# Kernel tuning notes

Measured on AMD Instinct MI355X. Metric: run time of the kernel, lower is better.

The kernel has to match this reference:

```python
import jax, jax.numpy as jnp
import numpy as np

DIM = 256
RADIUS = 3
DIAM = 2 * RADIUS + 1          # 7
NNEIGH = DIAM * DIAM           # 49
B, H, W = 2, 64, 64
EPS_LN = 1e-6
EPS_NORM = 1e-7


def conv1x1(x, w, b):
    # x: [B,Cin,H,W], w: [Cout,Cin], b: [Cout]
    return jnp.einsum('oi,bihw->bohw', w, x) + b[None, :, None, None]


def layernorm2d(x, g, b):
    # channel-wise norm as in LayerNorm2d (mean/var over channel dim)
    u = x.mean(1, keepdims=True)
    s = ((x - u) ** 2).mean(1, keepdims=True)
    xn = (x - u) / jnp.sqrt(s + EPS_LN)
    return g[None, :, None, None] * xn + b[None, :, None, None]


def unfold_reflect(x, r):
    # torch F.unfold(pad(x, reflect, r), kernel=2r+1).reshape(B,C,D*D,H,W)
    d = 2 * r + 1
    hh, ww = x.shape[2], x.shape[3]
    xp = jnp.pad(x, ((0, 0), (0, 0), (r, r), (r, r)), mode='reflect')
    pats = [xp[:, :, i:i + hh, j:j + ww] for i in range(d) for j in range(d)]
    return jnp.stack(pats, axis=2)  # [B,C,D*D,H,W]


def setup_inputs() -> dict:
    key = jax.random.key(0)
    ks = jax.random.split(key, 20)
    sc_c = 1.0 / np.sqrt(DIM)
    sc_f = 1.0 / np.sqrt(NNEIGH + DIM)
    inp = {
        'spatial_feats': jax.random.normal(ks[0], (B, DIM, H, W), jnp.float32),
        'semantic_feats': jax.random.normal(ks[1], (B, DIM, H, W), jnp.float32),
        # range_proj: conv1x1 -> LN2d -> SiLU -> conv1x1
        'rp_w1': jax.random.normal(ks[2], (DIM, DIM), jnp.float32) * sc_c,
        'rp_b1': jnp.zeros((DIM,), jnp.float32),
        'rp_g': jnp.ones((DIM,), jnp.float32),
        'rp_be': jnp.zeros((DIM,), jnp.float32),
        'rp_w2': jax.random.normal(ks[3], (DIM, DIM), jnp.float32) * sc_c,
        'rp_b2': jnp.zeros((DIM,), jnp.float32),
        # fixup_proj: conv1x1(49+C->49) -> LN2d -> SiLU -> conv1x1(49->49)
        'fp_w1': jax.random.normal(ks[4], (NNEIGH, NNEIGH + DIM), jnp.float32) * sc_f,
        'fp_b1': jnp.zeros((NNEIGH,), jnp.float32),
        'fp_g': jnp.ones((NNEIGH,), jnp.float32),
        'fp_be': jnp.zeros((NNEIGH,), jnp.float32),
        'fp_w2': jax.random.normal(ks[5], (NNEIGH, NNEIGH), jnp.float32) * (1.0 / np.sqrt(NNEIGH)),
        'fp_b2': jnp.zeros((NNEIGH,), jnp.float32),
        # output_proj: conv1x1 -> LN2d -> conv1x1
        'op_w1': jax.random.normal(ks[6], (DIM, DIM), jnp.float32) * sc_c,
        'op_b1': jnp.zeros((DIM,), jnp.float32),
        'op_g': jnp.ones((DIM,), jnp.float32),
        'op_be': jnp.zeros((DIM,), jnp.float32),
        'op_w2': jax.random.normal(ks[7], (DIM, DIM), jnp.float32) * sc_c,
        'op_b2': jnp.zeros((DIM,), jnp.float32),
        'sigma_spatial': jnp.ones((), jnp.float32),
    }
    return inp


def reference(spatial_feats, semantic_feats,
              rp_w1, rp_b1, rp_g, rp_be, rp_w2, rp_b2,
              fp_w1, fp_b1, fp_g, fp_be, fp_w2, fp_b2,
              op_w1, op_b1, op_g, op_be, op_w2, op_b2,
              sigma_spatial):
    scale = jnp.asarray(DIM ** 0.5, spatial_feats.dtype)
    # range_proj(semantic_feats)
    px = conv1x1(semantic_feats, rp_w1, rp_b1)
    px = jax.nn.silu(layernorm2d(px, rp_g, rp_be))
    px = conv1x1(px, rp_w2, rp_b2)  # [B,C,H,W]

    # spatial (Gaussian) kernel over the window
    lin = jnp.linspace(-1.0, 1.0, DIAM)
    xg, yg = jnp.meshgrid(lin, lin, indexing='ij')
    spatial_kernel = jnp.exp(-(xg ** 2 + yg ** 2) / (2.0 * sigma_spatial ** 2))
    spatial_kernel = spatial_kernel.reshape(1, NNEIGH, 1, 1)

    # range kernel: local similarity + softmax over the 49 neighbors
    queries = unfold_reflect(px, RADIUS)                       # [B,C,N,H,W]
    sim = jnp.einsum('bcnhw,bchw->bnhw', queries, px) / scale
    range_kernel = jax.nn.softmax(sim.astype(jnp.float32), axis=1).astype(px.dtype)

    # neighborhoods of spatial features
    neighborhoods = unfold_reflect(spatial_feats, RADIUS)      # [B,C,N,H,W]

    # gated fixup correction
    ck = range_kernel * spatial_kernel                          # [B,N,H,W]
    fx = conv1x1(jnp.concatenate([ck, semantic_feats], axis=1), fp_w1, fp_b1)
    fx = jax.nn.silu(layernorm2d(fx, fp_g, fp_be))
    fx = conv1x1(fx, fp_w2, fp_b2)
    ck = ck + ck * jax.nn.sigmoid(fx)
    ck = ck / (ck.sum(1, keepdims=True) + EPS_NORM)

    # weighted neighborhood sum
    out = jnp.einsum('bcnhw,bnhw->bchw', neighborhoods, ck)

    # output_proj (note: no SiLU here, matching the module)
    out = conv1x1(out, op_w1, op_b1)
    out = layernorm2d(out, op_g, op_be)
    out = conv1x1(out, op_w2, op_b2)
    return out
```

## Files before the change

### kernel.cpp

```cpp
#include <hip/hip_runtime.h>
#include <cstdint>

#define HW 4096
#define C_ 256
#define NN 49
#define KW 305

typedef __bf16 bf16;
typedef bf16 bf16x8 __attribute__((ext_vector_type(8)));
typedef bf16 bf16x4 __attribute__((ext_vector_type(4)));
typedef float f32x4 __attribute__((ext_vector_type(4)));

#define GLD16(src, dst) __builtin_amdgcn_global_load_lds( \
    (const __attribute__((address_space(1))) uint32_t*)(src), \
    (__attribute__((address_space(3))) uint32_t*)(dst), 16, 0, 0)

__device__ __forceinline__ int refl(int i) { return i < 0 ? -i : (i > 63 ? 126 - i : i); }
__device__ __forceinline__ float sigmoidf_(float x) { return 1.f / (1.f + __expf(-x)); }

__global__ __launch_bounds__(256) void setup_k(const float* __restrict__ spatial,
                                               const float* __restrict__ semantic,
                                               const float* __restrict__ rp_w1,
                                               const float* __restrict__ rp_w2,
                                               const float* __restrict__ op_w1,
                                               const float* __restrict__ op_w2,
                                               const float* __restrict__ fp_w1,
                                               const float* __restrict__ fp_w2,
                                               const float* __restrict__ sigma,
                                               bf16* __restrict__ spb, bf16* __restrict__ seb,
                                               bf16* __restrict__ wrp1, bf16* __restrict__ wrp2,
                                               bf16* __restrict__ wop1, bf16* __restrict__ wop2,
                                               bf16* __restrict__ w1ckb, bf16* __restrict__ w1sb,
                                               bf16* __restrict__ w2Tg, float* __restrict__ sk)
{
    __shared__ float tile[32][33];
    const int bid = blockIdx.x, t = threadIdx.x;
    if (bid < 4096) {
        int z = bid >> 10, r = bid & 1023;
        int b = z & 1;
        const float* src = (z >> 1) ? semantic : spatial;
        bf16* dst = (z >> 1) ? seb : spb;
        int p0 = (r & 127) * 32, c0 = (r >> 7) * 32;
        int tx = t & 31, ty = t >> 5;
        const float* s = src + (size_t)b * C_ * HW;
        #pragma unroll
        for (int i = 0; i < 32; i += 8)
            tile[ty + i][tx] = s[(size_t)(c0 + ty + i) * HW + p0 + tx];
        __syncthreads();
        int p = t >> 3, cq = (t & 7) * 4;
        bf16x4 o = {(bf16)tile[cq][p], (bf16)tile[cq + 1][p], (bf16)tile[cq + 2][p], (bf16)tile[cq + 3][p]};
        *(bf16x4*)&dst[((size_t)b * HW + p0 + p) * C_ + c0 + cq] = o;
        return;
    }
    int pid = bid - 4096;
    if (pid < 256) {
        const float* src = (pid < 64) ? rp_w1 : (pid < 128) ? rp_w2 : (pid < 192) ? op_w1 : op_w2;
        bf16* dst = (pid < 64) ? wrp1 : (pid < 128) ? wrp2 : (pid < 192) ? wop1 : wop2;
        int i = ((pid & 63) * 256 + t) * 4;
        f32x4 v = *(const f32x4*)&src[i];
        bf16x4 o = {(bf16)v[0], (bf16)v[1], (bf16)v[2], (bf16)v[3]};
        *(bf16x4*)&dst[i] = o;
    } else if (pid == 256) {
        if (t < NN) {
            int i = t / 7, j = t % 7;
            float xg = (i - 3) * (1.f / 3.f), yg = (j - 3) * (1.f / 3.f);
            float s = sigma[0];
            sk[t] = __expf(-(xg * xg + yg * yg) / (2.f * s * s));
        }
    } else if (pid < 270) {
        int idx = (pid - 257) * 256 + t;
        if (idx < NN * 64) {
            int k = idx >> 6, o = idx & 63;
            w1ckb[idx] = (o < NN) ? (bf16)fp_w1[o * KW + k] : (bf16)0.f;
        }
    } else if (pid < 334) {
        int idx = (pid - 270) * 256 + t;
        int o = idx >> 8, c = idx & 255;
        w1sb[idx] = (o < NN) ? (bf16)fp_w1[o * KW + NN + c] : (bf16)0.f;
    } else {
        int idx = (pid - 334) * 256 + t;
        if (idx < NN * 64) {
            int k = idx >> 6, o = idx & 63;
            w2Tg[idx] = (o < NN) ? (bf16)fp_w2[o * NN + k] : (bf16)0.f;
        }
    }
}

__device__ __forceinline__ void stage_b(const bf16* __restrict__ Wp, bf16* dst, int kc, int t)
{
    const bf16* gB = Wp + (size_t)(t >> 2) * C_ + kc + (((t & 3) ^ ((t >> 3) & 3)) * 8);
    #pragma unroll
    for (int ii = 0; ii < 4; ++ii)
        GLD16(gB + (size_t)ii * 64 * C_, dst + ii * 2048 + t * 8);
}

template<bool SILU, int MODE>
__global__ __launch_bounds__(256) void conv_pair(const bf16* __restrict__ X,
                                                 const bf16* __restrict__ W1,
                                                 const float* __restrict__ b1v,
                                                 const float* __restrict__ g,
                                                 const float* __restrict__ be,
                                                 const bf16* __restrict__ W2,
                                                 const float* __restrict__ b2v,
                                                 void* __restrict__ Yv)
{
    __shared__ __align__(16) bf16 Xf[32 * 256];
    __shared__ __align__(16) bf16 Mid[32 * 256];
    __shared__ __align__(16) bf16 Bs[2][256 * 32];
    __shared__ float lnred[32][4][2];
    const int t = threadIdx.x;
    const int lane = t & 63, wc = t >> 6;
    const int l15 = lane & 15, kb = lane >> 4;
    const long q0 = (long)blockIdx.x * 32;

    {
        const int r8 = t >> 5, slot = t & 31;
        const bf16* gX = X + (q0 + r8) * C_ + ((slot ^ (r8 & 7)) * 8);
        #pragma unroll
        for (int i = 0; i < 4; ++i)
            GLD16(gX + (size_t)i * 8 * C_, &Xf[i * 2048 + t * 8]);
    }
    stage_b(W1, &Bs[0][0], 0, t);

    const int x7 = l15 & 7;
    const int bsl = (kb ^ ((l15 >> 1) & 3)) * 8;
    int boff[4];
    #pragma unroll
    for (int n = 0; n < 4; ++n)
        boff[n] = (wc * 64 + n * 16 + l15) * 32 + bsl;
    const int a0base = l15 * 256;
    const int a1base = (16 + l15) * 256;

    f32x4 acc[2][4];
    #pragma unroll
    for (int m = 0; m < 2; ++m)
        #pragma unroll
        for (int n = 0; n < 4; ++n) acc[m][n] = (f32x4){0.f, 0.f, 0.f, 0.f};

    __syncthreads();
    int cur = 0;
    #pragma unroll
    for (int ks = 0; ks < 8; ++ks) {
        if (ks < 7) stage_b(W1, &Bs[cur ^ 1][0], (ks + 1) * 32, t);
        const int ko = ((ks * 4 + kb) ^ x7) * 8;
        bf16x8 a0 = *(const bf16x8*)&Xf[a0base + ko];
        bf16x8 a1 = *(const bf16x8*)&Xf[a1base + ko];
        #pragma unroll
        for (int n = 0; n < 4; ++n) {
            bf16x8 b = *(const bf16x8*)&Bs[cur][boff[n]];
            acc[0][n] = __builtin_amdgcn_mfma_f32_16x16x32_bf16(a0, b, acc[0][n], 0, 0, 0);
            acc[1][n] = __builtin_amdgcn_mfma_f32_16x16x32_bf16(a1, b, acc[1][n], 0, 0, 0);
        }
        __syncthreads();
        cur ^= 1;
    }

    stage_b(W2, &Bs[0][0], 0, t);

    float s4[2][4], ss4[2][4];
    #pragma unroll
    for (int m = 0; m < 2; ++m)
        #pragma unroll
        for (int r = 0; r < 4; ++r) { s4[m][r] = 0.f; ss4[m][r] = 0.f; }
    #pragma unroll
    for (int n = 0; n < 4; ++n) {
        float bo = b1v[wc * 64 + n * 16 + l15];
        #pragma unroll
        for (int m = 0; m < 2; ++m)
            #pragma unroll
            for (int r = 0; r < 4; ++r) {
                float v = acc[m][n][r] + bo;
                acc[m][n][r] = v;
                s4[m][r] += v; ss4[m][r] += v * v;
            }
    }
    #pragma unroll
    for (int off = 1; off <= 8; off <<= 1)
        #pragma unroll
        for (int m = 0; m < 2; ++m)
            #pragma unroll
            for (int r = 0; r < 4; ++r) {
                s4[m][r]  += __shfl_xor(s4[m][r], off, 64);
                ss4[m][r] += __shfl_xor(ss4[m][r], off, 64);
            }
    if (l15 == 0) {
        #pragma unroll
        for (int m = 0; m < 2; ++m)
            #pragma unroll
            for (int r = 0; r < 4; ++r) {
                lnred[m * 16 + kb * 4 + r][wc][0] = s4[m][r];
                lnred[m * 16 + kb * 4 + r][wc][1] = ss4[m][r];
            }
    }
    __syncthreads();
    float mean[2][4], rstd[2][4];
    #pragma unroll
    for (int m = 0; m < 2; ++m)
        #pragma unroll
        for (int r = 0; r < 4; ++r) {
            int p = m * 16 + kb * 4 + r;
            float st  = lnred[p][0][0] + lnred[p][1][0] + lnred[p][2][0] + lnred[p][3][0];
            float sst = lnred[p][0][1] + lnred[p][1][1] + lnred[p][2][1] + lnred[p][3][1];
            mean[m][r] = st * (1.f / 256.f);
            float var = sst * (1.f / 256.f) - mean[m][r] * mean[m][r];
            rstd[m][r] = rsqrtf(var + 1e-6f);
        }
    #pragma unroll
    for (int n = 0; n < 4; ++n) {
        int ch = wc * 64 + n * 16 + l15;
        float gv = g[ch], bev = be[ch];
        #pragma unroll
        for (int m = 0; m < 2; ++m)
            #pragma unroll
            for (int r = 0; r < 4; ++r) {
                float y = (acc[m][n][r] - mean[m][r]) * rstd[m][r] * gv + bev;
                if (SILU) y *= sigmoidf_(y);
                int p = m * 16 + kb * 4 + r;
                Mid[p * 256 + (((ch >> 3) ^ (p & 7)) * 8) + (ch & 7)] = (bf16)y;
            }
    }
    __syncthreads();

    f32x4 acc2[2][4];
    #pragma unroll
    for (int m = 0; m < 2; ++m)
        #pragma unroll
        for (int n = 0; n < 4; ++n) acc2[m][n] = (f32x4){0.f, 0.f, 0.f, 0.f};
    cur = 0;
    #pragma unroll
    for (int ks = 0; ks < 8; ++ks) {
        if (ks < 7) stage_b(W2, &Bs[cur ^ 1][0], (ks + 1) * 32, t);
        const int ko = ((ks * 4 + kb) ^ x7) * 8;
        bf16x8 a0 = *(const bf16x8*)&Mid[a0base + ko];
        bf16x8 a1 = *(const bf16x8*)&Mid[a1base + ko];
        #pragma unroll
        for (int n = 0; n < 4; ++n) {
            bf16x8 b = *(const bf16x8*)&Bs[cur][boff[n]];
            acc2[0][n] = __builtin_amdgcn_mfma_f32_16x16x32_bf16(a0, b, acc2[0][n], 0, 0, 0);
            acc2[1][n] = __builtin_amdgcn_mfma_f32_16x16x32_bf16(a1, b, acc2[1][n], 0, 0, 0);
        }
        __syncthreads();
        cur ^= 1;
    }

    if constexpr (MODE == 0) {
        #pragma unroll
        for (int n = 0; n < 4; ++n) {
            int ch = wc * 64 + n * 16 + l15;
            float bo = b2v[ch];
            #pragma unroll
            for (int m = 0; m < 2; ++m)
                #pragma unroll
                for (int r = 0; r < 4; ++r)
                    Xf[(m * 16 + kb * 4 + r) * 256 + ch] = (bf16)(acc2[m][n][r] + bo);
        }
        __syncthreads();
        bf16* Y = (bf16*)Yv;
        const int p = t >> 3, cb = (t & 7) * 32;
        #pragma unroll
        for (int i = 0; i < 4; ++i) {
            bf16x8 v = *(const bf16x8*)&Xf[p * 256 + cb + i * 8];
            *(bf16x8*)&Y[(q0 + p) * C_ + cb + i * 8] = v;
        }
    } else {
        float* Y = (float*)Yv;
        const int bb = (int)(q0 >> 12);
        #pragma unroll
        for (int n = 0; n < 4; ++n) {
            int ch = wc * 64 + n * 16 + l15;
            float bo = b2v[ch];
            #pragma unroll
            for (int m = 0; m < 2; ++m) {
                int pp = (int)(q0 & 4095) + m * 16 + kb * 4;
                f32x4 val = {acc2[m][n][0] + bo, acc2[m][n][1] + bo,
                             acc2[m][n][2] + bo, acc2[m][n][3] + bo};
                *(f32x4*)&Y[((size_t)bb * C_ + ch) * HW + pp] = val;
            }
        }
    }
}

__global__ __launch_bounds__(256) void attn_out_k(const bf16* __restrict__ px,
                                                  const bf16* __restrict__ spb,
                                                  const bf16* __restrict__ seb,
                                                  const bf16* __restrict__ w1sb,
                                                  const bf16* __restrict__ w1ckb,
                                                  const bf16* __restrict__ w2Tg,
                                                  const float* __restrict__ b1,
                                                  const float* __restrict__ b2,
                                                  const float* __restrict__ g,
                                                  const float* __restrict__ be,
                                                  const float* __restrict__ sk,
                                                  const bf16* __restrict__ wop1,
                                                  const float* __restrict__ ob1,
                                                  const float* __restrict__ og,
                                                  const float* __restrict__ obe,
                                                  const bf16* __restrict__ wop2,
                                                  const float* __restrict__ ob2,
                                                  float* __restrict__ Y)
{
    __shared__ __align__(16) char shm[49664];
    bf16*  uni = (bf16*)(shm);
    float* ckl = (float*)(shm + 25600);
    float* hb  = (float*)(shm + 29760);
    float* S   = (float*)(shm + 32768);
    float* fxs = (float*)(shm + 40384);
    bf16*  Xg  = (bf16*)(shm + 32768);
    bf16*  Mid = (bf16*)(shm + 40960);
    bf16*  Bs0 = (bf16*)(shm);
    bf16*  Bs1 = (bf16*)(shm + 16384);
    float* lnred = (float*)(shm + 49152);

    const int t = threadIdx.x, lane = t & 63, wid = t >> 6;
    const int l15 = lane & 15, kb = lane >> 4;
    const int blk = blockIdx.x;
    const int batch = blk >> 8, tt = blk & 255;
    const int h0 = (tt >> 4) * 4, w0 = (tt & 15) * 4;
    const long base = (long)batch * HW;

    const float bo  = (lane < NN) ? b1[lane] : 0.f;
    const float gl  = (lane < NN) ? g[lane] : 0.f;
    const float bel = (lane < NN) ? be[lane] : 0.f;
    const float b2l = (lane < NN) ? b2[lane] : 0.f;
    const float skv = (lane < NN) ? sk[lane] : 0.f;
    const int nn_ = (lane < NN) ? lane : 0;
    const int dy = nn_ / 7, dx = nn_ % 7;

#define STAGE_UNI(ci) do { \
    _Pragma("unroll") \
    for (int i_ = 0; i_ < 7; ++i_) { \
        int st_ = i_ * 256 + t; \
        if (st_ < 1600) { \
            int u_ = st_ >> 4, s_ = st_ & 15; \
            int uy_ = (u_ * 205) >> 11, ux_ = u_ - uy_ * 10; \
            long grow_ = base + refl(h0 + uy_ - 3) * 64 + refl(w0 + ux_ - 3); \
            GLD16(spb + grow_ * C_ + (ci) * 128 + ((s_ ^ (u_ & 7)) * 8), &uni[u_ * 128 + s_ * 8]); \
        } \
    } \
} while (0)

    STAGE_UNI(0);

    const int ppy = l15 >> 2, ppx = l15 & 3;
    const long qB = base + (h0 + ppy) * 64 + (w0 + ppx);
    const bf16* bpxp = px + qB * C_ + kb * 8;
    const bf16* bsemp = seb + qB * C_ + kb * 8;

    bool valid[3], ispx[3];
    const bf16* arow[3];
    #pragma unroll
    for (int j = 0; j < 3; ++j) {
        int tid = wid + 4 * j;
        valid[j] = tid < 11;
        ispx[j] = tid < 7;
        int u = tid * 16 + l15;
        int uy = (u * 205) >> 11, ux = u - uy * 10;
        long grow = (u < 100) ? base + refl(h0 + uy - 3) * 64 + refl(w0 + ux - 3) : base;
        int o = ((tid - 7) & 3) * 16 + l15;
        arow[j] = ispx[j] ? (px + grow * C_ + kb * 8)
                          : (w1sb + (size_t)o * C_ + kb * 8);
    }

    f32x4 acc[3];
    #pragma unroll
    for (int j = 0; j < 3; ++j) acc[j] = (f32x4){0.f, 0.f, 0.f, 0.f};

    #pragma unroll
    for (int ks = 0; ks < 8; ++ks) {
        bf16x8 bp = *(const bf16x8*)(bpxp + ks * 32);
        bf16x8 bs = *(const bf16x8*)(bsemp + ks * 32);
        #pragma unroll
        for (int j = 0; j < 3; ++j) {
            if (valid[j]) {
                bf16x8 a = *(const bf16x8*)(arow[j] + ks * 32);
                acc[j] = __builtin_amdgcn_mfma_f32_16x16x32_bf16(a, ispx[j] ? bp : bs, acc[j], 0, 0, 0);
            }
        }
    }

    float w1r[NN], w2r[NN];
    #pragma unroll
    for (int k = 0; k < NN; ++k) {
        w1r[k] = (float)w1ckb[k * 64 + lane];
        w2r[k] = (float)w2Tg[k * 64 + lane];
    }

    #pragma unroll
    for (int j = 0; j < 3; ++j) {
        if (valid[j]) {
            int tid = wid + 4 * j;
            float* dst = ispx[j] ? &S[(tid * 16 + kb * 4) * 17 + l15]
                                 : &fxs[(((tid - 7) * 16) + kb * 4) * 17 + l15];
            dst[0] = acc[j][0]; dst[17] = acc[j][1]; dst[34] = acc[j][2]; dst[51] = acc[j][3];
        }
    }
    __syncthreads();

    #pragma unroll
    for (int j = 0; j < 4; ++j) {
        int p = wid * 4 + j, py = p >> 2, px4 = p & 3;
        int u = (py + dy) * 10 + px4 + dx;
        float sval = (lane < NN) ? S[u * 17 + p] * 0.0625f : -1e30f;
        float mx = sval;
        #pragma unroll
        for (int off = 32; off; off >>= 1) mx = fmaxf(mx, __shfl_xor(mx, off, 64));
        float ev = (lane < NN) ? __expf(sval - mx) : 0.f;
        float ssum = ev;
        #pragma unroll
        for (int off = 32; off; off >>= 1) ssum += __shfl_xor(ssum, off, 64);
        ckl[p * 65 + lane] = (lane < NN) ? (ev / ssum) * skv : 0.f;
    }

    #pragma unroll
    for (int j = 0; j < 4; ++j) {
        int p = wid * 4 + j;
        float fxa = 0.f, fxb = 0.f;
        #pragma unroll
        for (int k = 0; k < 48; k += 2) {
            fxa += w1r[k] * ckl[p * 65 + k];
            fxb += w1r[k + 1] * ckl[p * 65 + k + 1];
        }
        fxa += w1r[48] * ckl[p * 65 + 48];
        float fx = fxs[lane * 17 + p] + bo + fxa + fxb;
        float s = fx, ss = fx * fx;
        #pragma unroll
        for (int off = 32; off; off >>= 1) {
            s  += __shfl_xor(s, off, 64);
            ss += __shfl_xor(ss, off, 64);
        }
        float mean = s * (1.f / 49.f);
        float var  = ss * (1.f / 49.f) - mean * mean;
        float rstd = rsqrtf(var + 1e-6f);
        float hv = 0.f;
        if (lane < NN) {
            float xn = (fx - mean) * rstd * gl + bel;
            hv = xn * sigmoidf_(xn);
        }
        hb[wid * 64 + lane] = hv;
        float ckv = 0.f;
        if (lane < NN) {
            float ca = 0.f, cb = 0.f;
            #pragma unroll
            for (int k = 0; k < 48; k += 2) {
                ca += w2r[k] * hb[wid * 64 + k];
                cb += w2r[k + 1] * hb[wid * 64 + k + 1];
            }
            ca += w2r[48] * hb[wid * 64 + 48];
            ckv = ckl[p * 65 + lane] * (1.f + sigmoidf_(b2l + ca + cb));
        }
        float tot = ckv;
        #pragma unroll
        for (int off = 32; off; off >>= 1) tot += __shfl_xor(tot, off, 64);
        ckl[p * 65 + lane] = (lane < NN) ? ckv / (tot + 1e-7f) : 0.f;
    }
    __syncthreads();

    const int sub = lane >> 4;
    const int gp = wid * 4 + sub;

    #pragma unroll
    for (int ci = 0; ci < 2; ++ci) {
        if (ci == 1) {
            __syncthreads();
            STAGE_UNI(1);
            __syncthreads();
        }
        const int ub = (gp >> 2) * 10 + (gp & 3);
        float a[8];
        #pragma unroll
        for (int e = 0; e < 8; ++e) a[e] = 0.f;
        for (int dyy = 0; dyy < 7; ++dyy) {
            bf16x8 v[7];
            #pragma unroll
            for (int dxx = 0; dxx < 7; ++dxx) {
                int u = ub + dyy * 10 + dxx;
                v[dxx] = *(const bf16x8*)&uni[u * 128 + ((l15 ^ (u & 7)) * 8)];
            }
            #pragma unroll
            for (int dxx = 0; dxx < 7; ++dxx) {
                float cv = ckl[gp * 65 + dyy * 7 + dxx];
                #pragma unroll
                for (int e = 0; e < 8; ++e) a[e] += cv * (float)v[dxx][e];
            }
        }
        bf16x8 ov;
        #pragma unroll
        for (int e = 0; e < 8; ++e) ov[e] = (bf16)a[e];
        *(bf16x8*)&Xg[gp * 256 + (((ci * 16 + l15) ^ (gp & 7)) * 8)] = ov;
    }
    __syncthreads();

    stage_b(wop1, Bs0, 0, t);

    const int x7 = l15 & 7;
    const int bsl = (kb ^ ((l15 >> 1) & 3)) * 8;
    int boff[4];
    #pragma unroll
    for (int n = 0; n < 4; ++n)
        boff[n] = (wid * 64 + n * 16 + l15) * 32 + bsl;

    f32x4 cacc[4];
    #pragma unroll
    for (int n = 0; n < 4; ++n) cacc[n] = (f32x4){0.f, 0.f, 0.f, 0.f};

    __syncthreads();
    int cur = 0;
    #pragma unroll
    for (int ks = 0; ks < 8; ++ks) {
        if (ks < 7) stage_b(wop1, cur ? Bs0 : Bs1, (ks + 1) * 32, t);
        const int ko = ((ks * 4 + kb) ^ x7) * 8;
        bf16x8 a = *(const bf16x8*)&Xg[l15 * 256 + ko];
        #pragma unroll
        for (int n = 0; n < 4; ++n) {
            bf16x8 b = *(const bf16x8*)&((cur ? Bs1 : Bs0)[boff[n]]);
            cacc[n] = __builtin_amdgcn_mfma_f32_16x16x32_bf16(a, b, cacc[n], 0, 0, 0);
        }
        __syncthreads();
        cur ^= 1;
    }

    stage_b(wop2, Bs0, 0, t);

    float s4[4] = {0.f, 0.f, 0.f, 0.f}, ss4[4] = {0.f, 0.f, 0.f, 0.f};
    #pragma unroll
    for (int n = 0; n < 4; ++n) {
        float bv = ob1[wid * 64 + n * 16 + l15];
        #pragma unroll
        for (int r = 0; r < 4; ++r) {
            float v = cacc[n][r] + bv;
            cacc[n][r] = v;
            s4[r] += v; ss4[r] += v * v;
        }
    }
    #pragma unroll
    for (int off = 1; off <= 8; off <<= 1)
        #pragma unroll
        for (int r = 0; r < 4; ++r) {
            s4[r]  += __shfl_xor(s4[r], off, 64);
            ss4[r] += __shfl_xor(ss4[r], off, 64);
        }
    if (l15 == 0) {
        #pragma unroll
        for (int r = 0; r < 4; ++r) {
            lnred[((kb * 4 + r) * 4 + wid) * 2 + 0] = s4[r];
            lnred[((kb * 4 + r) * 4 + wid) * 2 + 1] = ss4[r];
        }
    }
    __syncthreads();
    float mean[4], rstd[4];
    #pragma unroll
    for (int r = 0; r < 4; ++r) {
        int p = kb * 4 + r;
        float st  = lnred[(p * 4 + 0) * 2] + lnred[(p * 4 + 1) * 2] + lnred[(p * 4 + 2) * 2] + lnred[(p * 4 + 3) * 2];
        float sst = lnred[(p * 4 + 0) * 2 + 1] + lnred[(p * 4 + 1) * 2 + 1] + lnred[(p * 4 + 2) * 2 + 1] + lnred[(p * 4 + 3) * 2 + 1];
        mean[r] = st * (1.f / 256.f);
        float var = sst * (1.f / 256.f) - mean[r] * mean[r];
        rstd[r] = rsqrtf(var + 1e-6f);
    }
    #pragma unroll
    for (int n = 0; n < 4; ++n) {
        int ch = wid * 64 + n * 16 + l15;
        float gv = og[ch], bev = obe[ch];
        #pragma unroll
        for (int r = 0; r < 4; ++r) {
            float y = (cacc[n][r] - mean[r]) * rstd[r] * gv + bev;
            int p = kb * 4 + r;
            Mid[p * 256 + (((ch >> 3) ^ (p & 7)) * 8) + (ch & 7)] = (bf16)y;
        }
    }
    __syncthreads();

    f32x4 cacc2[4];
    #pragma unroll
    for (int n = 0; n < 4; ++n) cacc2[n] = (f32x4){0.f, 0.f, 0.f, 0.f};
    cur = 0;
    #pragma unroll
    for (int ks = 0; ks < 8; ++ks) {
        if (ks < 7) stage_b(wop2, cur ? Bs0 : Bs1, (ks + 1) * 32, t);
        const int ko = ((ks * 4 + kb) ^ x7) * 8;
        bf16x8 a = *(const bf16x8*)&Mid[l15 * 256 + ko];
        #pragma unroll
        for (int n = 0; n < 4; ++n) {
            bf16x8 b = *(const bf16x8*)&((cur ? Bs1 : Bs0)[boff[n]]);
            cacc2[n] = __builtin_amdgcn_mfma_f32_16x16x32_bf16(a, b, cacc2[n], 0, 0, 0);
        }
        __syncthreads();
        cur ^= 1;
    }

    {
        const size_t rowbase = ((size_t)batch * C_) * HW + (size_t)(h0 + kb) * 64 + w0;
        #pragma unroll
        for (int n = 0; n < 4; ++n) {
            int ch = wid * 64 + n * 16 + l15;
            float bv = ob2[ch];
            f32x4 val = {cacc2[n][0] + bv, cacc2[n][1] + bv, cacc2[n][2] + bv, cacc2[n][3] + bv};
            *(f32x4*)&Y[rowbase + (size_t)ch * HW] = val;
        }
    }
#undef STAGE_UNI
}

extern "C" void kernel_launch(void* const* d_in, const int* in_sizes, int n_in,
                              void* d_out, int out_size, void* d_ws, size_t ws_size,
                              hipStream_t stream)
{
    const float* spatial  = (const float*)d_in[0];
    const float* semantic = (const float*)d_in[1];
    const float* rp_w1 = (const float*)d_in[2];
    const float* rp_b1 = (const float*)d_in[3];
    const float* rp_g  = (const float*)d_in[4];
    const float* rp_be = (const float*)d_in[5];
    const float* rp_w2 = (const float*)d_in[6];
    const float* rp_b2 = (const float*)d_in[7];
    const float* fp_w1 = (const float*)d_in[8];
    const float* fp_b1 = (const float*)d_in[9];
    const float* fp_g  = (const float*)d_in[10];
    const float* fp_be = (const float*)d_in[11];
    const float* fp_w2 = (const float*)d_in[12];
    const float* fp_b2 = (const float*)d_in[13];
    const float* op_w1 = (const float*)d_in[14];
    const float* op_b1 = (const float*)d_in[15];
    const float* op_g  = (const float*)d_in[16];
    const float* op_be = (const float*)d_in[17];
    const float* op_w2 = (const float*)d_in[18];
    const float* op_b2 = (const float*)d_in[19];
    const float* sigma = (const float*)d_in[20];

    const size_t NPX = 2 * (size_t)HW;
    float* ws = (float*)d_ws;
    float* sk    = ws;
    bf16* bfbase = (bf16*)(sk + 64);
    bf16* spb = bfbase;
    bf16* seb = spb + NPX * C_;
    bf16* t1  = seb + NPX * C_;
    bf16* wrp1 = t1 + NPX * C_;
    bf16* wrp2 = wrp1 + C_ * C_;
    bf16* wop1 = wrp2 + C_ * C_;
    bf16* wop2 = wop1 + C_ * C_;
    bf16* w1sb = wop2 + C_ * C_;
    bf16* w2Tg = w1sb + 64 * C_;
    bf16* w1ckb = w2Tg + 3200;

    setup_k<<<4443, 256, 0, stream>>>(spatial, semantic, rp_w1, rp_w2, op_w1, op_w2,
                                      fp_w1, fp_w2, sigma,
                                      spb, seb, wrp1, wrp2, wop1, wop2,
                                      w1ckb, w1sb, w2Tg, sk);

    conv_pair<true, 0><<<256, 256, 0, stream>>>(seb, wrp1, rp_b1, rp_g, rp_be, wrp2, rp_b2, t1);

    attn_out_k<<<512, 256, 0, stream>>>(t1, spb, seb, w1sb, w1ckb, w2Tg, fp_b1, fp_b2,
                                        fp_g, fp_be, sk,
                                        wop1, op_b1, op_g, op_be, wop2, op_b2,
                                        (float*)d_out);
}
```

Before: 65.74 us.

## Double attn_out_k block to 512 threads and read neighborhoods straight from global

The fused attention/output kernel now runs 8 waves per block instead of 4. Each wave handles half as many pixels and output-channel tiles. The fixup weights w1/w2 are staged into LDS instead of being held in 98 registers per thread, which lowers register pressure. The weighted neighborhood sum loads spatial features directly from global memory (relying on cache) instead of staging the 10x10 halo into LDS in two channel halves, which removes those staging passes and their barriers. In exchange it does more uncached-path global loads and pays for reductions across more waves.

Measured after the change: 70.59 us. +7.4%, slower.

```diff
diff --git a/kernel.cpp b/kernel.cpp
--- a/kernel.cpp
+++ b/kernel.cpp
@@ -94,6 +94,13 @@
         GLD16(gB + (size_t)ii * 64 * C_, dst + ii * 2048 + t * 8);
 }
 
+__device__ __forceinline__ void stage_b512(const bf16* __restrict__ Wp, bf16* dst, int kc, int t)
+{
+    const bf16* gB = Wp + (size_t)(t >> 2) * C_ + kc + (((t & 3) ^ ((t >> 3) & 3)) * 8);
+    GLD16(gB, dst + t * 8);
+    GLD16(gB + (size_t)128 * C_, dst + 4096 + t * 8);
+}
+
 template<bool SILU, int MODE>
 __global__ __launch_bounds__(256) void conv_pair(const bf16* __restrict__ X,
                                                  const bf16* __restrict__ W1,
@@ -280,39 +287,40 @@
     }
 }
 
-__global__ __launch_bounds__(256) void attn_out_k(const bf16* __restrict__ px,
-                                                  const bf16* __restrict__ spb,
-                                                  const bf16* __restrict__ seb,
-                                                  const bf16* __restrict__ w1sb,
-                                                  const bf16* __restrict__ w1ckb,
-                                                  const bf16* __restrict__ w2Tg,
-                                                  const float* __restrict__ b1,
-                                                  const float* __restrict__ b2,
-                                                  const float* __restrict__ g,
-                                                  const float* __restrict__ be,
-                                                  const float* __restrict__ sk,
-                                                  const bf16* __restrict__ wop1,
-                                                  const float* __restrict__ ob1,
-                                                  const float* __restrict__ og,
-                                                  const float* __restrict__ obe,
-                                                  const bf16* __restrict__ wop2,
-                                                  const float* __restrict__ ob2,
-                                                  float* __restrict__ Y)
+__global__ __launch_bounds__(512, 4) void attn_out_k(const bf16* __restrict__ px,
+                                                     const bf16* __restrict__ spb,
+                                                     const bf16* __restrict__ seb,
+                                                     const bf16* __restrict__ w1sb,
+                                                     const bf16* __restrict__ w1ckb,
+                                                     const bf16* __restrict__ w2Tg,
+                                                     const float* __restrict__ b1,
+                                                     const float* __restrict__ b2,
+                                                     const float* __restrict__ g,
+                                                     const float* __restrict__ be,
+                                                     const float* __restrict__ sk,
+                                                     const bf16* __restrict__ wop1,
+                                                     const float* __restrict__ ob1,
+                                                     const float* __restrict__ og,
+                                                     const float* __restrict__ obe,
+                                                     const bf16* __restrict__ wop2,
+                                                     const float* __restrict__ ob2,
+                                                     float* __restrict__ Y)
 {
-    __shared__ __align__(16) char shm[49664];
-    bf16*  uni = (bf16*)(shm);
-    float* ckl = (float*)(shm + 25600);
-    float* hb  = (float*)(shm + 29760);
-    float* S   = (float*)(shm + 32768);
-    float* fxs = (float*)(shm + 40384);
-    bf16*  Xg  = (bf16*)(shm + 32768);
-    bf16*  Mid = (bf16*)(shm + 40960);
-    bf16*  Bs0 = (bf16*)(shm);
-    bf16*  Bs1 = (bf16*)(shm + 16384);
-    float* lnred = (float*)(shm + 49152);
+    __shared__ __align__(16) char shm[56384];
+    float* ckl = (float*)(shm);
+    float* hb  = (float*)(shm + 4160);
+    float* S   = (float*)(shm + 6208);
+    float* fxs = (float*)(shm + 13824);
+    bf16*  w1l = (bf16*)(shm + 18176);
+    bf16*  w2l = (bf16*)(shm + 24448);
+    bf16*  Bs0 = (bf16*)(shm + 6208);
+    bf16*  Bs1 = (bf16*)(shm + 22592);
+    bf16*  Xg  = (bf16*)(shm + 38976);
+    bf16*  Mid = (bf16*)(shm + 47168);
+    float* lnred = (float*)(shm + 55360);
 
     const int t = threadIdx.x, lane = t & 63, wid = t >> 6;
-    const int l15 = lane & 15, kb = lane >> 4;
+    const int l15 = lane & 15, kb = lane >> 4, l31 = lane & 31;
     const int blk = blockIdx.x;
     const int batch = blk >> 8, tt = blk & 255;
     const int h0 = (tt >> 4) * 4, w0 = (tt & 15) * 4;
@@ -326,79 +334,52 @@
     const int nn_ = (lane < NN) ? lane : 0;
     const int dy = nn_ / 7, dx = nn_ % 7;
 
-#define STAGE_UNI(ci) do { \
-    _Pragma("unroll") \
-    for (int i_ = 0; i_ < 7; ++i_) { \
-        int st_ = i_ * 256 + t; \
-        if (st_ < 1600) { \
-            int u_ = st_ >> 4, s_ = st_ & 15; \
-            int uy_ = (u_ * 205) >> 11, ux_ = u_ - uy_ * 10; \
-            long grow_ = base + refl(h0 + uy_ - 3) * 64 + refl(w0 + ux_ - 3); \
-            GLD16(spb + grow_ * C_ + (ci) * 128 + ((s_ ^ (u_ & 7)) * 8), &uni[u_ * 128 + s_ * 8]); \
-        } \
-    } \
-} while (0)
-
-    STAGE_UNI(0);
+    if (t < 392) GLD16(w1ckb + (size_t)t * 8, &w1l[t * 8]);
+    if (t < 392) GLD16(w2Tg + (size_t)t * 8, &w2l[t * 8]);
 
     const int ppy = l15 >> 2, ppx = l15 & 3;
     const long qB = base + (h0 + ppy) * 64 + (w0 + ppx);
     const bf16* bpxp = px + qB * C_ + kb * 8;
     const bf16* bsemp = seb + qB * C_ + kb * 8;
 
-    bool valid[3], ispx[3];
-    const bf16* arow[3];
-    #pragma unroll
-    for (int j = 0; j < 3; ++j) {
-        int tid = wid + 4 * j;
-        valid[j] = tid < 11;
-        ispx[j] = tid < 7;
-        int u = tid * 16 + l15;
+    const bool t0sim = wid < 7;
+    const bool t1v = wid < 3;
+    const bf16* a0p;
+    {
+        int u = wid * 16 + l15;
         int uy = (u * 205) >> 11, ux = u - uy * 10;
         long grow = (u < 100) ? base + refl(h0 + uy - 3) * 64 + refl(w0 + ux - 3) : base;
-        int o = ((tid - 7) & 3) * 16 + l15;
-        arow[j] = ispx[j] ? (px + grow * C_ + kb * 8)
-                          : (w1sb + (size_t)o * C_ + kb * 8);
-    }
-
-    f32x4 acc[3];
-    #pragma unroll
-    for (int j = 0; j < 3; ++j) acc[j] = (f32x4){0.f, 0.f, 0.f, 0.f};
-
+        a0p = t0sim ? (px + grow * C_ + kb * 8)
+                    : (w1sb + (size_t)l15 * C_ + kb * 8);
+    }
+    const bf16* a1p = w1sb + (size_t)((wid + 1) * 16 + l15) * C_ + kb * 8;
+
+    f32x4 acc0 = {0.f, 0.f, 0.f, 0.f}, acc1 = {0.f, 0.f, 0.f, 0.f};
     #pragma unroll
     for (int ks = 0; ks < 8; ++ks) {
         bf16x8 bp = *(const bf16x8*)(bpxp + ks * 32);
         bf16x8 bs = *(const bf16x8*)(bsemp + ks * 32);
-        #pragma unroll
-        for (int j = 0; j < 3; ++j) {
-            if (valid[j]) {
-                bf16x8 a = *(const bf16x8*)(arow[j] + ks * 32);
-                acc[j] = __builtin_amdgcn_mfma_f32_16x16x32_bf16(a, ispx[j] ? bp : bs, acc[j], 0, 0, 0);
-            }
-        }
-    }
-
-    float w1r[NN], w2r[NN];
-    #pragma unroll
-    for (int k = 0; k < NN; ++k) {
-        w1r[k] = (float)w1ckb[k * 64 + lane];
-        w2r[k] = (float)w2Tg[k * 64 + lane];
-    }
-
-    #pragma unroll
-    for (int j = 0; j < 3; ++j) {
-        if (valid[j]) {
-            int tid = wid + 4 * j;
-            float* dst = ispx[j] ? &S[(tid * 16 + kb * 4) * 17 + l15]
-                                 : &fxs[(((tid - 7) * 16) + kb * 4) * 17 + l15];
-            dst[0] = acc[j][0]; dst[17] = acc[j][1]; dst[34] = acc[j][2]; dst[51] = acc[j][3];
-        }
-    }
-    __syncthreads();
-
-    #pragma unroll
-    for (int j = 0; j < 4; ++j) {
-        int p = wid * 4 + j, py = p >> 2, px4 = p & 3;
+        bf16x8 a0 = *(const bf16x8*)(a0p + ks * 32);
+        acc0 = __builtin_amdgcn_mfma_f32_16x16x32_bf16(a0, t0sim ? bp : bs, acc0, 0, 0, 0);
+        if (t1v) {
+            bf16x8 a1 = *(const bf16x8*)(a1p + ks * 32);
+            acc1 = __builtin_amdgcn_mfma_f32_16x16x32_bf16(a1, bs, acc1, 0, 0, 0);
+        }
+    }
+    {
+        float* dst = t0sim ? &S[(wid * 16 + kb * 4) * 17 + l15]
+                           : &fxs[(kb * 4) * 17 + l15];
+        dst[0] = acc0[0]; dst[17] = acc0[1]; dst[34] = acc0[2]; dst[51] = acc0[3];
+    }
+    if (t1v) {
+        float* dst = &fxs[((wid + 1) * 16 + kb * 4) * 17 + l15];
+        dst[0] = acc1[0]; dst[17] = acc1[1]; dst[34] = acc1[2]; dst[51] = acc1[3];
+    }
+    __syncthreads();
+
+    #pragma unroll
+    for (int j = 0; j < 2; ++j) {
+        int p = wid * 2 + j, py = p >> 2, px4 = p & 3;
         int u = (py + dy) * 10 + px4 + dx;
         float sval = (lane < NN) ? S[u * 17 + p] * 0.0625f : -1e30f;
         float mx = sval;
@@ -412,15 +393,15 @@
     }
 
     #pragma unroll
-    for (int j = 0; j < 4; ++j) {
-        int p = wid * 4 + j;
+    for (int j = 0; j < 2; ++j) {
+        int p = wid * 2 + j;
         float fxa = 0.f, fxb = 0.f;
         #pragma unroll
         for (int k = 0; k < 48; k += 2) {
-            fxa += w1r[k] * ckl[p * 65 + k];
-            fxb += w1r[k + 1] * ckl[p * 65 + k + 1];
-        }
-        fxa += w1r[48] * ckl[p * 65 + 48];
+            fxa += (float)w1l[k * 64 + lane] * ckl[p * 65 + k];
+            fxb += (float)w1l[(k + 1) * 64 + lane] * ckl[p * 65 + k + 1];
+        }
+        fxa += (float)w1l[48 * 64 + lane] * ckl[p * 65 + 48];
         float fx = fxs[lane * 17 + p] + bo + fxa + fxb;
         float s = fx, ss = fx * fx;
         #pragma unroll
@@ -442,10 +423,10 @@
             float ca = 0.f, cb = 0.f;
             #pragma unroll
             for (int k = 0; k < 48; k += 2) {
-                ca += w2r[k] * hb[wid * 64 + k];
-                cb += w2r[k + 1] * hb[wid * 64 + k + 1];
+                ca += (float)w2l[k * 64 + lane] * hb[wid * 64 + k];
+                cb += (float)w2l[(k + 1) * 64 + lane] * hb[wid * 64 + k + 1];
             }
-            ca += w2r[48] * hb[wid * 64 + 48];
+            ca += (float)w2l[48 * 64 + lane] * hb[wid * 64 + 48];
             ckv = ckl[p * 65 + lane] * (1.f + sigmoidf_(b2l + ca + cb));
         }
         float tot = ckv;
@@ -455,27 +436,27 @@
     }
     __syncthreads();
 
-    const int sub = lane >> 4;
-    const int gp = wid * 4 + sub;
-
-    #pragma unroll
-    for (int ci = 0; ci < 2; ++ci) {
-        if (ci == 1) {
-            __syncthreads();
-            STAGE_UNI(1);
-            __syncthreads();
-        }
-        const int ub = (gp >> 2) * 10 + (gp & 3);
+    stage_b512(wop1, Bs0, 0, t);
+
+    {
+        const int gp = wid * 2 + (lane >> 5);
+        const int gpy = gp >> 2, gpx = gp & 3;
+        int ry[7], rx[7];
+        #pragma unroll
+        for (int d = 0; d < 7; ++d) {
+            ry[d] = refl(h0 + gpy + d - 3) * 64;
+            rx[d] = refl(w0 + gpx + d - 3);
+        }
+        const bf16* pb = spb + base * C_ + l31 * 8;
         float a[8];
         #pragma unroll
         for (int e = 0; e < 8; ++e) a[e] = 0.f;
+        #pragma unroll
         for (int dyy = 0; dyy < 7; ++dyy) {
             bf16x8 v[7];
             #pragma unroll
-            for (int dxx = 0; dxx < 7; ++dxx) {
-                int u = ub + dyy * 10 + dxx;
-                v[dxx] = *(const bf16x8*)&uni[u * 128 + ((l15 ^ (u & 7)) * 8)];
-            }
+            for (int dxx = 0; dxx < 7; ++dxx)
+                v[dxx] = *(const bf16x8*)(pb + (size_t)(ry[dyy] + rx[dxx]) * C_);
             #pragma unroll
             for (int dxx = 0; dxx < 7; ++dxx) {
                 float cv = ckl[gp * 65 + dyy * 7 + dxx];
@@ -486,32 +467,29 @@
         bf16x8 ov;
         #pragma unroll
         for (int e = 0; e < 8; ++e) ov[e] = (bf16)a[e];
-        *(bf16x8*)&Xg[gp * 256 + (((ci * 16 + l15) ^ (gp & 7)) * 8)] = ov;
-    }
-    __syncthreads();
-
-    stage_b(wop1, Bs0, 0, t);
+        *(bf16x8*)&Xg[gp * 256 + ((l31 ^ (gp & 7)) * 8)] = ov;
+    }
+    __syncthreads();
 
     const int x7 = l15 & 7;
     const int bsl = (kb ^ ((l15 >> 1) & 3)) * 8;
-    int boff[4];
-    #pragma unroll
-    for (int n = 0; n < 4; ++n)
-        boff[n] = (wid * 64 + n * 16 + l15) * 32 + bsl;
-
-    f32x4 cacc[4];
-    #pragma unroll
-    for (int n = 0; n < 4; ++n) cacc[n] = (f32x4){0.f, 0.f, 0.f, 0.f};
-
-    __syncthreads();
+    int boff[2];
+    #pragma unroll
+    for (int n = 0; n < 2; ++n)
+        boff[n] = (wid * 32 + n * 16 + l15) * 32 + bsl;
+
+    f32x4 cacc[2];
+    #pragma unroll
+    for (int n = 0; n < 2; ++n) cacc[n] = (f32x4){0.f, 0.f, 0.f, 0.f};
+
     int cur = 0;
     #pragma unroll
     for (int ks = 0; ks < 8; ++ks) {
-        if (ks < 7) stage_b(wop1, cur ? Bs0 : Bs1, (ks + 1) * 32, t);
+        if (ks < 7) stage_b512(wop1, cur ? Bs0 : Bs1, (ks + 1) * 32, t);
         const int ko = ((ks * 4 + kb) ^ x7) * 8;
         bf16x8 a = *(const bf16x8*)&Xg[l15 * 256 + ko];
         #pragma unroll
-        for (int n = 0; n < 4; ++n) {
+        for (int n = 0; n < 2; ++n) {
             bf16x8 b = *(const bf16x8*)&((cur ? Bs1 : Bs0)[boff[n]]);
             cacc[n] = __builtin_amdgcn_mfma_f32_16x16x32_bf16(a, b, cacc[n], 0, 0, 0);
         }
@@ -519,12 +497,12 @@
         cur ^= 1;
     }
 
-    stage_b(wop2, Bs0, 0, t);
+    stage_b512(wop2, Bs0, 0, t);
 
     float s4[4] = {0.f, 0.f, 0.f, 0.f}, ss4[4] = {0.f, 0.f, 0.f, 0.f};
     #pragma unroll
-    for (int n = 0; n < 4; ++n) {
-        float bv = ob1[wid * 64 + n * 16 + l15];
+    for (int n = 0; n < 2; ++n) {
+        float bv = ob1[wid * 32 + n * 16 + l15];
         #pragma unroll
         for (int r = 0; r < 4; ++r) {
             float v = cacc[n][r] + bv;
@@ -542,8 +520,8 @@
     if (l15 == 0) {
         #pragma unroll
         for (int r = 0; r < 4; ++r) {
-            lnred[((kb * 4 + r) * 4 + wid) * 2 + 0] = s4[r];
-            lnred[((kb * 4 + r) * 4 + wid) * 2 + 1] = ss4[r];
+            lnred[((kb * 4 + r) * 8 + wid) * 2 + 0] = s4[r];
+            lnred[((kb * 4 + r) * 8 + wid) * 2 + 1] = ss4[r];
         }
     }
     __syncthreads();
@@ -551,15 +529,19 @@
     #pragma unroll
     for (int r = 0; r < 4; ++r) {
         int p = kb * 4 + r;
-        float st  = lnred[(p * 4 + 0) * 2] + lnred[(p * 4 + 1) * 2] + lnred[(p * 4 + 2) * 2] + lnred[(p * 4 + 3) * 2];
-        float sst = lnred[(p * 4 + 0) * 2 + 1] + lnred[(p * 4 + 1) * 2 + 1] + lnred[(p * 4 + 2) * 2 + 1] + lnred[(p * 4 + 3) * 2 + 1];
+        float st = 0.f, sst = 0.f;
+        #pragma unroll
+        for (int w = 0; w < 8; ++w) {
+            st  += lnred[(p * 8 + w) * 2 + 0];
+            sst += lnred[(p * 8 + w) * 2 + 1];
+        }
         mean[r] = st * (1.f / 256.f);
         float var = sst * (1.f / 256.f) - mean[r] * mean[r];
         rstd[r] = rsqrtf(var + 1e-6f);
     }
     #pragma unroll
-    for (int n = 0; n < 4; ++n) {
-        int ch = wid * 64 + n * 16 + l15;
+    for (int n = 0; n < 2; ++n) {
+        int ch = wid * 32 + n * 16 + l15;
         float gv = og[ch], bev = obe[ch];
         #pragma unroll
         for (int r = 0; r < 4; ++r) {
@@ -570,17 +552,17 @@
     }
     __syncthreads();
 
-    f32x4 cacc2[4];
-    #pragma unroll
-    for (int n = 0; n < 4; ++n) cacc2[n] = (f32x4){0.f, 0.f, 0.f, 0.f};
+    f32x4 cacc2[2];
+    #pragma unroll
+    for (int n = 0; n < 2; ++n) cacc2[n] = (f32x4){0.f, 0.f, 0.f, 0.f};
     cur = 0;
     #pragma unroll
     for (int ks = 0; ks < 8; ++ks) {
-        if (ks < 7) stage_b(wop2, cur ? Bs0 : Bs1, (ks + 1) * 32, t);
+        if (ks < 7) stage_b512(wop2, cur ? Bs0 : Bs1, (ks + 1) * 32, t);
         const int ko = ((ks * 4 + kb) ^ x7) * 8;
         bf16x8 a = *(const bf16x8*)&Mid[l15 * 256 + ko];
         #pragma unroll
-        for (int n = 0; n < 4; ++n) {
+        for (int n = 0; n < 2; ++n) {
             bf16x8 b = *(const bf16x8*)&((cur ? Bs1 : Bs0)[boff[n]]);
             cacc2[n] = __builtin_amdgcn_mfma_f32_16x16x32_bf16(a, b, cacc2[n], 0, 0, 0);
         }
@@ -591,14 +573,13 @@
     {
         const size_t rowbase = ((size_t)batch * C_) * HW + (size_t)(h0 + kb) * 64 + w0;
         #pragma unroll
-        for (int n = 0; n < 4; ++n) {
-            int ch = wid * 64 + n * 16 + l15;
+        for (int n = 0; n < 2; ++n) {
+            int ch = wid * 32 + n * 16 + l15;
             float bv = ob2[ch];
             f32x4 val = {cacc2[n][0] + bv, cacc2[n][1] + bv, cacc2[n][2] + bv, cacc2[n][3] + bv};
             *(f32x4*)&Y[rowbase + (size_t)ch * HW] = val;
         }
     }
-#undef STAGE_UNI
 }
 
 extern "C" void kernel_launch(void* const* d_in, const int* in_sizes, int n_in,
@@ -649,7 +630,7 @@
 
     conv_pair<true, 0><<<256, 256, 0, stream>>>(seb, wrp1, rp_b1, rp_g, rp_be, wrp2, rp_b2, t1);
 
-    attn_out_k<<<512, 256, 0, stream>>>(t1, spb, seb, w1sb, w1ckb, w2Tg, fp_b1, fp_b2,
+    attn_out_k<<<512, 512, 0, stream>>>(t1, spb, seb, w1sb, w1ckb, w2Tg, fp_b1, fp_b2,
                                         fp_g, fp_be, sk,
                                         wop1, op_b1, op_g, op_be, wop2, op_b2,
                                         (float*)d_out);
```

## Stage full-channel spatial halo once in LDS and overlap weight staging

Applied to the files above, without the earlier changes.

The 10x10 halo of spatial features used for the weighted neighborhood sum is now staged for all 256 channels in a single up-front async load, instead of two 128-channel halves with a mid-kernel reload and barriers. Each lane now covers 32 channel groups for two pixels at a time, and the first output-projection weight tile is staged before the neighborhood sum so that load overlaps the compute. Shared memory per block grows from about 49 KB to about 72 KB, which may reduce the number of resident blocks per CU. The XOR swizzle on halo reads is also dropped, which may introduce LDS bank conflicts.

After: 64.86 us, median of 3. No clear change (-1.3%).

```diff
diff --git a/kernel.cpp b/kernel.cpp
--- a/kernel.cpp
+++ b/kernel.cpp
@@ -299,20 +299,20 @@
                                                   const float* __restrict__ ob2,
                                                   float* __restrict__ Y)
 {
-    __shared__ __align__(16) char shm[49664];
+    __shared__ __align__(16) char shm[72768];
     bf16*  uni = (bf16*)(shm);
-    float* ckl = (float*)(shm + 25600);
-    float* hb  = (float*)(shm + 29760);
-    float* S   = (float*)(shm + 32768);
-    float* fxs = (float*)(shm + 40384);
-    bf16*  Xg  = (bf16*)(shm + 32768);
-    bf16*  Mid = (bf16*)(shm + 40960);
-    bf16*  Bs0 = (bf16*)(shm);
+    float* ckl = (float*)(shm + 51200);
+    float* hb  = (float*)(shm + 55360);
+    float* S   = (float*)(shm + 56384);
+    float* fxs = (float*)(shm + 64000);
+    bf16*  Bs0 = (bf16*)(shm + 56384);
     bf16*  Bs1 = (bf16*)(shm + 16384);
-    float* lnred = (float*)(shm + 49152);
+    bf16*  Xg  = (bf16*)(shm);
+    bf16*  Mid = (bf16*)(shm + 32768);
+    float* lnred = (float*)(shm + 40960);
 
     const int t = threadIdx.x, lane = t & 63, wid = t >> 6;
-    const int l15 = lane & 15, kb = lane >> 4;
+    const int l15 = lane & 15, kb = lane >> 4, l31 = lane & 31;
     const int blk = blockIdx.x;
     const int batch = blk >> 8, tt = blk & 255;
     const int h0 = (tt >> 4) * 4, w0 = (tt & 15) * 4;
@@ -326,20 +326,16 @@
     const int nn_ = (lane < NN) ? lane : 0;
     const int dy = nn_ / 7, dx = nn_ % 7;
 
-#define STAGE_UNI(ci) do { \
-    _Pragma("unroll") \
-    for (int i_ = 0; i_ < 7; ++i_) { \
-        int st_ = i_ * 256 + t; \
-        if (st_ < 1600) { \
-            int u_ = st_ >> 4, s_ = st_ & 15; \
-            int uy_ = (u_ * 205) >> 11, ux_ = u_ - uy_ * 10; \
-            long grow_ = base + refl(h0 + uy_ - 3) * 64 + refl(w0 + ux_ - 3); \
-            GLD16(spb + grow_ * C_ + (ci) * 128 + ((s_ ^ (u_ & 7)) * 8), &uni[u_ * 128 + s_ * 8]); \
-        } \
-    } \
-} while (0)
-
-    STAGE_UNI(0);
+    #pragma unroll
+    for (int i = 0; i < 13; ++i) {
+        int st = i * 256 + t;
+        if (st < 3200) {
+            int u = st >> 5, s = st & 31;
+            int uy = (u * 205) >> 11, ux = u - uy * 10;
+            long grow = base + refl(h0 + uy - 3) * 64 + refl(w0 + ux - 3);
+            GLD16(spb + grow * C_ + s * 8, &uni[u * 256 + s * 8]);
+        }
+    }
 
     const int ppy = l15 >> 2, ppx = l15 & 3;
     const long qB = base + (h0 + ppy) * 64 + (w0 + ppx);
@@ -455,26 +451,23 @@
     }
     __syncthreads();
 
-    const int sub = lane >> 4;
-    const int gp = wid * 4 + sub;
-
-    #pragma unroll
-    for (int ci = 0; ci < 2; ++ci) {
-        if (ci == 1) {
-            __syncthreads();
-            STAGE_UNI(1);
-            __syncthreads();
-        }
+    stage_b(wop1, Bs0, 0, t);
+
+    bf16x8 ov[2];
+    #pragma unroll
+    for (int j = 0; j < 2; ++j) {
+        const int gp = wid * 4 + j * 2 + (lane >> 5);
         const int ub = (gp >> 2) * 10 + (gp & 3);
         float a[8];
         #pragma unroll
         for (int e = 0; e < 8; ++e) a[e] = 0.f;
+        #pragma unroll
         for (int dyy = 0; dyy < 7; ++dyy) {
             bf16x8 v[7];
             #pragma unroll
             for (int dxx = 0; dxx < 7; ++dxx) {
                 int u = ub + dyy * 10 + dxx;
-                v[dxx] = *(const bf16x8*)&uni[u * 128 + ((l15 ^ (u & 7)) * 8)];
+                v[dxx] = *(const bf16x8*)&uni[u * 256 + l31 * 8];
             }
             #pragma unroll
             for (int dxx = 0; dxx < 7; ++dxx) {
@@ -483,14 +476,17 @@
                 for (int e = 0; e < 8; ++e) a[e] += cv * (float)v[dxx][e];
             }
         }
-        bf16x8 ov;
-        #pragma unroll
-        for (int e = 0; e < 8; ++e) ov[e] = (bf16)a[e];
-        *(bf16x8*)&Xg[gp * 256 + (((ci * 16 + l15) ^ (gp & 7)) * 8)] = ov;
-    }
-    __syncthreads();
-
-    stage_b(wop1, Bs0, 0, t);
+        #pragma unroll
+        for (int e = 0; e < 8; ++e) ov[j][e] = (bf16)a[e];
+    }
+    __syncthreads();
+
+    #pragma unroll
+    for (int j = 0; j < 2; ++j) {
+        const int gp = wid * 4 + j * 2 + (lane >> 5);
+        *(bf16x8*)&Xg[gp * 256 + ((l31 ^ (gp & 7)) * 8)] = ov[j];
+    }
+    __syncthreads();
 
     const int x7 = l15 & 7;
     const int bsl = (kb ^ ((l15 >> 1) & 3)) * 8;
@@ -503,7 +499,6 @@
     #pragma unroll
     for (int n = 0; n < 4; ++n) cacc[n] = (f32x4){0.f, 0.f, 0.f, 0.f};
 
-    __syncthreads();
     int cur = 0;
     #pragma unroll
     for (int ks = 0; ks < 8; ++ks) {
@@ -598,7 +593,6 @@
             *(f32x4*)&Y[rowbase + (size_t)ch * HW] = val;
         }
     }
-#undef STAGE_UNI
 }
 
 extern "C" void kernel_launch(void* const* d_in, const int* in_sizes, int n_in,
```
